# Kernel tuning notes

Measured on AMD Instinct MI355X. Metric: run time of the kernel, lower is better.

Reference implementation:

```python
import jax, jax.numpy as jnp
import numpy as np

N = 50000   # nodes
E = 800000  # edges
IN, HID, HEADS, OUT = 128, 32, 4, 64
NEG_SLOPE = 0.2


def _gatv2_layer(x, src, dst, Wl, bl, Wr, br, att, bias, res_W, concat):
    """One PyG-style GATv2Conv layer (eval mode, no dropout).
    x: [N, F_in]; att: [H, C]. Returns [N, H*C] if concat else [N, C]."""
    H, C = att.shape
    xl = (x @ Wl + bl).reshape(N, H, C)   # source transform
    xr = (x @ Wr + br).reshape(N, H, C)   # target transform
    e = jax.nn.leaky_relu(xl[src] + xr[dst], NEG_SLOPE)        # [E, H, C]
    logit = jnp.einsum('ehc,hc->eh', e, att)                   # [E, H]
    # segment softmax over incoming edges per destination node
    m = jax.ops.segment_max(logit, dst, num_segments=N)        # [N, H]
    p = jnp.exp(logit - m[dst])
    denom = jax.ops.segment_sum(p, dst, num_segments=N)
    alpha = p / (denom[dst] + 1e-16)                           # [E, H]
    out = jax.ops.segment_sum(xl[src] * alpha[:, :, None], dst, num_segments=N)  # [N, H, C]
    out = out.reshape(N, H * C) if concat else out.mean(axis=1)
    if res_W is not None:
        out = out + x @ res_W
    return out + bias


def _glorot(key, shape):
    fan_in = shape[0] if len(shape) > 1 else shape[-1]
    return jax.random.normal(key, shape, dtype=jnp.float32) / np.sqrt(fan_in)


def setup_inputs() -> dict:
    key = jax.random.key(0)
    ks = iter(jax.random.split(key, 32))
    x = jax.random.normal(next(ks), (N, IN), dtype=jnp.float32)
    edge_index = jax.random.randint(next(ks), (2, E), 0, N, dtype=jnp.int64)
    d = {"x": x, "edge_index": edge_index}
    HC = HEADS * HID  # 128
    # layer 0: IN -> HEADS*HID, concat, residual
    d["Wl0"] = _glorot(next(ks), (IN, HC)); d["bl0"] = jnp.zeros((HC,), jnp.float32)
    d["Wr0"] = _glorot(next(ks), (IN, HC)); d["br0"] = jnp.zeros((HC,), jnp.float32)
    d["att0"] = _glorot(next(ks), (HEADS, HID)); d["b0"] = jnp.zeros((HC,), jnp.float32)
    d["res0"] = _glorot(next(ks), (IN, HC))
    # layer 1: HC -> HEADS*HID, concat, residual
    d["Wl1"] = _glorot(next(ks), (HC, HC)); d["bl1"] = jnp.zeros((HC,), jnp.float32)
    d["Wr1"] = _glorot(next(ks), (HC, HC)); d["br1"] = jnp.zeros((HC,), jnp.float32)
    d["att1"] = _glorot(next(ks), (HEADS, HID)); d["b1"] = jnp.zeros((HC,), jnp.float32)
    d["res1"] = _glorot(next(ks), (HC, HC))
    # layer 2: HC -> OUT, heads=1, concat=False, no residual
    d["Wl2"] = _glorot(next(ks), (HC, OUT)); d["bl2"] = jnp.zeros((OUT,), jnp.float32)
    d["Wr2"] = _glorot(next(ks), (HC, OUT)); d["br2"] = jnp.zeros((OUT,), jnp.float32)
    d["att2"] = _glorot(next(ks), (1, OUT)); d["b2"] = jnp.zeros((OUT,), jnp.float32)
    return d


def reference(x, edge_index,
              Wl0, bl0, Wr0, br0, att0, b0, res0,
              Wl1, bl1, Wr1, br1, att1, b1, res1,
              Wl2, bl2, Wr2, br2, att2, b2):
    src, dst = edge_index[0], edge_index[1]
    h = _gatv2_layer(x, src, dst, Wl0, bl0, Wr0, br0, att0, b0, res0, True)
    h = jax.nn.elu(h)
    h = _gatv2_layer(h, src, dst, Wl1, bl1, Wr1, br1, att1, b1, res1, True)
    h = jax.nn.elu(h)
    return _gatv2_layer(h, src, dst, Wl2, bl2, Wr2, br2, att2, b2, None, False)
```

## Files before the change

kernel.cpp:

```cpp
#include <hip/hip_runtime.h>
#include <math.h>

#define NN 50000
#define EE 800000
#define NBK 196
#define EPB 4096

typedef short v8s __attribute__((ext_vector_type(8)));
typedef float v4f __attribute__((ext_vector_type(4)));
typedef float v16f __attribute__((ext_vector_type(16)));

__device__ __forceinline__ ushort f2bf(float f) {
    uint u = __float_as_uint(f);
    uint r = (u + 0x7fffu + ((u >> 16) & 1u)) >> 16;
    return (ushort)r;
}
__device__ __forceinline__ float bf2f(ushort h) {
    return __uint_as_float(((uint)h) << 16);
}
__device__ __forceinline__ float lrelu(float x) {
    return fmaf(0.4f, fabsf(x), 0.6f * x);
}

template <int CTRL>
__device__ __forceinline__ float dppadd(float x) {
    int y = __builtin_amdgcn_update_dpp(0, __float_as_int(x), CTRL, 0xf, 0xf, true);
    return x + __int_as_float(y);
}
__device__ __forceinline__ float sum8(float x) {
    x = dppadd<0xB1>(x);
    x = dppadd<0x4E>(x);
    x = dppadd<0x141>(x);
    return x;
}
__device__ __forceinline__ float sum16(float x) {
    x = sum8(x);
    x = dppadd<0x140>(x);
    return x;
}
__device__ __forceinline__ float expclamp(float t) {
    return __expf(fminf(fmaxf(t, -60.f), 80.f));
}

struct WPack {
    const float* W[8];
    ushort* Th[8];
    ushort* Tl[8];
    int fout[8];
};

__global__ __launch_bounds__(256) void k_build1(const int* __restrict__ edst,
                                                int* __restrict__ bcnt,
                                                WPack p) {
    int t = threadIdx.x;
    if (blockIdx.x < 196) {
        __shared__ int h[NBK];
        if (t < NBK) h[t] = 0;
        __syncthreads();
        int eb = blockIdx.x * EPB;
        #pragma unroll
        for (int k = 0; k < EPB / 256; ++k) {
            int e = eb + k * 256 + t;
            if (e < EE) atomicAdd(&h[edst[e] >> 8], 1);
        }
        __syncthreads();
        if (t < NBK && h[t]) atomicAdd(&bcnt[t], h[t]);
    } else {
        int bid = blockIdx.x - 196;
        int wi = bid >> 6;
        int ib = bid & 63;
        int fout = p.fout[wi];
        int total = 128 * fout;
        int i = ib * 256 + t;
        if (i >= total) return;
        int k = i / fout;
        int n = i - k * fout;
        float f = p.W[wi][i];
        ushort h = f2bf(f);
        float lo = f - bf2f(h);
        int tt = n >> 5, c32 = n & 31, c = k >> 4, khalf = (k >> 3) & 1, j = k & 7;
        int flat = (((tt * 8 + c) * 64) + khalf * 32 + c32) * 8 + j;
        p.Th[wi][flat] = h;
        p.Tl[wi][flat] = f2bf(lo);
    }
}

__global__ __launch_bounds__(256) void k_bktplace(const int* __restrict__ esrc,
                                                  const int* __restrict__ edst,
                                                  const int* __restrict__ bcnt,
                                                  int* __restrict__ gcur,
                                                  uint* __restrict__ ebuf) {
    __shared__ int sc[256];
    __shared__ int h[NBK];
    __shared__ int base[NBK];
    int t = threadIdx.x;
    int v = (t < NBK) ? bcnt[t] : 0;
    sc[t] = v;
    __syncthreads();
    for (int o = 1; o < 256; o <<= 1) {
        int a = (t >= o) ? sc[t - o] : 0;
        __syncthreads();
        sc[t] += a;
        __syncthreads();
    }
    int bexcl = sc[t] - v;
    if (t < NBK) h[t] = 0;
    __syncthreads();

    int eb = blockIdx.x * EPB;
    int pk[EPB / 256];
    #pragma unroll
    for (int k = 0; k < EPB / 256; ++k) {
        int e = eb + k * 256 + t;
        pk[k] = -1;
        if (e < EE) {
            int b = edst[e] >> 8;
            int r = atomicAdd(&h[b], 1);
            pk[k] = (b << 16) | r;
        }
    }
    __syncthreads();
    if (t < NBK && h[t]) base[t] = bexcl + atomicAdd(&gcur[t], h[t]);
    __syncthreads();
    #pragma unroll
    for (int k = 0; k < EPB / 256; ++k) {
        int e = eb + k * 256 + t;
        if (e < EE) {
            int b = pk[k] >> 16;
            int r = pk[k] & 0xFFFF;
            uint dl = (uint)(edst[e] & 255);
            ebuf[base[b] + r] = (dl << 16) | (uint)esrc[e];
        }
    }
}

__global__ __launch_bounds__(256) void k_bktfin(const uint* __restrict__ ebuf,
                                                const int* __restrict__ bcnt,
                                                int* __restrict__ rowptr,
                                                int* __restrict__ csrc) {
    __shared__ int sm[256];
    __shared__ int deg[256];
    __shared__ int cur[256];
    __shared__ int s_eb, s_ec;
    const int b = blockIdx.x;
    const int t = threadIdx.x;

    int v = (t < NBK) ? bcnt[t] : 0;
    sm[t] = v;
    deg[t] = 0;
    __syncthreads();
    for (int o = 1; o < 256; o <<= 1) {
        int a = (t >= o) ? sm[t - o] : 0;
        __syncthreads();
        sm[t] += a;
        __syncthreads();
    }
    if (t == b) { s_eb = sm[t] - v; s_ec = v; }
    __syncthreads();
    const int eb = s_eb;
    const int ec = s_ec;

    for (int k = t; k < ec; k += 256)
        atomicAdd(&deg[ebuf[eb + k] >> 16], 1);
    __syncthreads();
    int dv = deg[t];
    sm[t] = dv;
    __syncthreads();
    for (int o = 1; o < 256; o <<= 1) {
        int a = (t >= o) ? sm[t - o] : 0;
        __syncthreads();
        sm[t] += a;
        __syncthreads();
    }
    int node = b * 256 + t;
    if (node < NN) rowptr[node + 1] = eb + sm[t];
    if (node == 0) rowptr[0] = 0;
    cur[t] = sm[t] - dv;
    __syncthreads();
    for (int k = t; k < ec; k += 256) {
        uint u = ebuf[eb + k];
        int nl = (int)(u >> 16);
        int r = atomicAdd(&cur[nl], 1);
        csrc[eb + r] = (int)(u & 0xFFFFu);
    }
}

template <int FOUT, int NW, bool CVT>
__global__ __launch_bounds__(64) void k_gemm_mfma(
    const float* __restrict__ Xf,
    const ushort* __restrict__ Xh, const ushort* __restrict__ Xl,
    const ushort* __restrict__ T0h, const ushort* __restrict__ T0l, const float* __restrict__ B0,
    const ushort* __restrict__ T1h, const ushort* __restrict__ T1l, const float* __restrict__ B1,
    const ushort* __restrict__ T2h, const ushort* __restrict__ T2l,
    ushort* __restrict__ O0b, float* __restrict__ O1, float* __restrict__ O2)
{
    const int lane  = threadIdx.x & 63;
    const int c32   = lane & 31;
    const int khalf = lane >> 5;
    const int row0  = blockIdx.x * 32;

    const ushort* Th[3] = {T0h, T1h, T2h};
    const ushort* Tl[3] = {T0l, T1l, T2l};
    const float*  Bp[3] = {B0, B1, nullptr};

    v8s ah[8], al[8];
    {
        int arow = row0 + c32;
        if (arow > NN - 1) arow = NN - 1;
        #pragma unroll
        for (int c = 0; c < 8; ++c) {
            size_t off = (size_t)arow * 128 + c * 16 + khalf * 8;
            if constexpr (CVT) {
                float4 f0 = *(const float4*)(Xf + off);
                float4 f1 = *(const float4*)(Xf + off + 4);
                const float fe[8] = {f0.x, f0.y, f0.z, f0.w, f1.x, f1.y, f1.z, f1.w};
                #pragma unroll
                for (int e = 0; e < 8; ++e) {
                    ushort h = f2bf(fe[e]);
                    float lo = fe[e] - bf2f(h);
                    ah[c][e] = (short)h;
                    al[c][e] = (short)(__float_as_uint(lo) >> 16);
                }
            } else {
                ah[c] = *(const v8s*)(Xh + off);
                al[c] = *(const v8s*)(Xl + off);
            }
        }
    }

    #pragma unroll
    for (int w = 0; w < NW; ++w) {
        const ushort* th = Th[w];
        const ushort* tl = Tl[w];
        const float* bias = Bp[w];
        float* Of = (w == 1) ? O1 : O2;
        #pragma unroll
        for (int t = 0; t < FOUT / 32; ++t) {
            v16f acc = {0.f,0.f,0.f,0.f, 0.f,0.f,0.f,0.f, 0.f,0.f,0.f,0.f, 0.f,0.f,0.f,0.f};
            #pragma unroll
            for (int c = 0; c < 8; ++c) {
                int boff = ((t * 8 + c) * 64 + lane) * 8;
                v8s bh = *(const v8s*)(th + boff);
                v8s bl = *(const v8s*)(tl + boff);
                acc = __builtin_amdgcn_mfma_f32_32x32x16_bf16(al[c], bh, acc, 0, 0, 0);
                acc = __builtin_amdgcn_mfma_f32_32x32x16_bf16(ah[c], bl, acc, 0, 0, 0);
                acc = __builtin_amdgcn_mfma_f32_32x32x16_bf16(ah[c], bh, acc, 0, 0, 0);
            }
            const int col = t * 32 + c32;
            float badd = bias ? bias[col] : 0.f;
            if (w == 0) {
                #pragma unroll
                for (int reg = 0; reg < 16; ++reg) {
                    int r = row0 + (reg & 3) + 8 * (reg >> 2) + 4 * khalf;
                    if (r < NN) O0b[(size_t)r * FOUT + col] = f2bf(acc[reg] + badd);
                }
            } else {
                #pragma unroll
                for (int reg = 0; reg < 16; ++reg) {
                    int r = row0 + (reg & 3) + 8 * (reg >> 2) + 4 * khalf;
                    if (r < NN) Of[(size_t)r * FOUT + col] = acc[reg] + badd;
                }
            }
        }
    }
}

__global__ __launch_bounds__(256) void k_agg01(const ushort* __restrict__ XLb,
                                               const float4* __restrict__ XR4,
                                               const float4* __restrict__ RES4,
                                               const float* __restrict__ att,
                                               const float* __restrict__ bias,
                                               const int* __restrict__ rowptr,
                                               const int* __restrict__ csrc,
                                               ushort* __restrict__ Hh,
                                               ushort* __restrict__ Hl) {
    const int lane = threadIdx.x & 63;
    const int wid = threadIdx.x >> 6;
    const int n = blockIdx.x * 4 + wid;
    if (n >= NN) return;
    const int beg = rowptr[n];
    const int end = rowptr[n + 1];
    const int half = lane >> 5;
    const uint j = lane & 31;

    const float4 xr = XR4[(uint)n * 32u + j];
    const float4 at = ((const float4*)att)[j];
    float4 s = {0.f, 0.f, 0.f, 0.f};
    float d = 0.f;

    int i = beg;
    for (; i + 4 <= end; i += 4) {
        uint sa = (uint)csrc[i + half];
        uint sb = (uint)csrc[i + 2 + half];
        ushort4 ua = *(const ushort4*)(XLb + sa * 128u + 4u * j);
        ushort4 ub = *(const ushort4*)(XLb + sb * 128u + 4u * j);
        {
            float4 va = {bf2f(ua.x), bf2f(ua.y), bf2f(ua.z), bf2f(ua.w)};
            float t0 = lrelu(va.x + xr.x) * at.x;
            t0 = fmaf(lrelu(va.y + xr.y), at.y, t0);
            t0 = fmaf(lrelu(va.z + xr.z), at.z, t0);
            t0 = fmaf(lrelu(va.w + xr.w), at.w, t0);
            float p = expclamp(sum8(t0));
            d += p;
            s.x = fmaf(p, va.x, s.x); s.y = fmaf(p, va.y, s.y);
            s.z = fmaf(p, va.z, s.z); s.w = fmaf(p, va.w, s.w);
        }
        {
            float4 vb = {bf2f(ub.x), bf2f(ub.y), bf2f(ub.z), bf2f(ub.w)};
            float t0 = lrelu(vb.x + xr.x) * at.x;
            t0 = fmaf(lrelu(vb.y + xr.y), at.y, t0);
            t0 = fmaf(lrelu(vb.z + xr.z), at.z, t0);
            t0 = fmaf(lrelu(vb.w + xr.w), at.w, t0);
            float p = expclamp(sum8(t0));
            d += p;
            s.x = fmaf(p, vb.x, s.x); s.y = fmaf(p, vb.y, s.y);
            s.z = fmaf(p, vb.z, s.z); s.w = fmaf(p, vb.w, s.w);
        }
    }
    for (; i < end; i += 2) {
        int ia = i + half;
        if (ia > end - 1) ia = end - 1;
        uint sa = (uint)csrc[ia];
        ushort4 ua = *(const ushort4*)(XLb + sa * 128u + 4u * j);
        float4 va = {bf2f(ua.x), bf2f(ua.y), bf2f(ua.z), bf2f(ua.w)};
        float t0 = lrelu(va.x + xr.x) * at.x;
        t0 = fmaf(lrelu(va.y + xr.y), at.y, t0);
        t0 = fmaf(lrelu(va.z + xr.z), at.z, t0);
        t0 = fmaf(lrelu(va.w + xr.w), at.w, t0);
        float p = expclamp(sum8(t0));
        if (half && (i + 1 >= end)) p = 0.f;
        d += p;
        s.x = fmaf(p, va.x, s.x); s.y = fmaf(p, va.y, s.y);
        s.z = fmaf(p, va.z, s.z); s.w = fmaf(p, va.w, s.w);
    }

    d   += __shfl_xor(d, 32);
    s.x += __shfl_xor(s.x, 32);
    s.y += __shfl_xor(s.y, 32);
    s.z += __shfl_xor(s.z, 32);
    s.w += __shfl_xor(s.w, 32);

    if (half == 0) {
        float inv = (d > 0.f) ? 1.f / d : 0.f;
        float4 rv = RES4[(uint)n * 32u + j];
        float4 bv = ((const float4*)bias)[j];
        float o0 = fmaf(s.x, inv, rv.x + bv.x);
        float o1 = fmaf(s.y, inv, rv.y + bv.y);
        float o2 = fmaf(s.z, inv, rv.z + bv.z);
        float o3 = fmaf(s.w, inv, rv.w + bv.w);
        o0 = o0 > 0.f ? o0 : __expf(o0) - 1.f;
        o1 = o1 > 0.f ? o1 : __expf(o1) - 1.f;
        o2 = o2 > 0.f ? o2 : __expf(o2) - 1.f;
        o3 = o3 > 0.f ? o3 : __expf(o3) - 1.f;
        ushort4 h, l;
        h.x = f2bf(o0); l.x = f2bf(o0 - bf2f(h.x));
        h.y = f2bf(o1); l.y = f2bf(o1 - bf2f(h.y));
        h.z = f2bf(o2); l.z = f2bf(o2 - bf2f(h.z));
        h.w = f2bf(o3); l.w = f2bf(o3 - bf2f(h.w));
        *(ushort4*)(Hh + (uint)n * 128u + 4u * j) = h;
        *(ushort4*)(Hl + (uint)n * 128u + 4u * j) = l;
    }
}

__global__ __launch_bounds__(256) void k_agg2(const ushort* __restrict__ XLb,
                                              const float4* __restrict__ XR4,
                                              const float* __restrict__ att,
                                              const float* __restrict__ bias,
                                              const int* __restrict__ rowptr,
                                              const int* __restrict__ csrc,
                                              float* __restrict__ OUT) {
    const int lane = threadIdx.x & 63;
    const int wid = threadIdx.x >> 6;
    const int n = blockIdx.x * 4 + wid;
    if (n >= NN) return;
    const int beg = rowptr[n];
    const int end = rowptr[n + 1];
    const int q = lane >> 4;
    const uint jj = lane & 15;

    const float4 xr = XR4[(uint)n * 16u + jj];
    const float4 at = ((const float4*)att)[jj];
    float4 s = {0.f, 0.f, 0.f, 0.f};
    float d = 0.f;
    const int e1 = end - 1;

    for (int i = beg; i < end; i += 8) {
        int i0 = i + q;
        int i1 = i + 4 + q;
        uint s0 = (uint)csrc[min(i0, e1)];
        uint s1 = (uint)csrc[min(i1, e1)];
        ushort4 u0 = *(const ushort4*)(XLb + s0 * 64u + 4u * jj);
        ushort4 u1 = *(const ushort4*)(XLb + s1 * 64u + 4u * jj);
        #pragma unroll
        for (int u = 0; u < 2; ++u) {
            ushort4 uv = (u == 0) ? u0 : u1;
            int ii = (u == 0) ? i0 : i1;
            float4 v = {bf2f(uv.x), bf2f(uv.y), bf2f(uv.z), bf2f(uv.w)};
            float t0 = lrelu(v.x + xr.x) * at.x;
            t0 = fmaf(lrelu(v.y + xr.y), at.y, t0);
            t0 = fmaf(lrelu(v.z + xr.z), at.z, t0);
            t0 = fmaf(lrelu(v.w + xr.w), at.w, t0);
            float p = expclamp(sum16(t0));
            if (ii >= end) p = 0.f;
            d += p;
            s.x = fmaf(p, v.x, s.x); s.y = fmaf(p, v.y, s.y);
            s.z = fmaf(p, v.z, s.z); s.w = fmaf(p, v.w, s.w);
        }
    }

    d   += __shfl_xor(d, 16);   d   += __shfl_xor(d, 32);
    s.x += __shfl_xor(s.x, 16); s.x += __shfl_xor(s.x, 32);
    s.y += __shfl_xor(s.y, 16); s.y += __shfl_xor(s.y, 32);
    s.z += __shfl_xor(s.z, 16); s.z += __shfl_xor(s.z, 32);
    s.w += __shfl_xor(s.w, 16); s.w += __shfl_xor(s.w, 32);

    if (lane < 16) {
        float inv = (d > 0.f) ? 1.f / d : 0.f;
        float4 bv = ((const float4*)bias)[jj];
        float4 o;
        o.x = fmaf(s.x, inv, bv.x);
        o.y = fmaf(s.y, inv, bv.y);
        o.z = fmaf(s.z, inv, bv.z);
        o.w = fmaf(s.w, inv, bv.w);
        *(float4*)(OUT + (uint)n * 64u + 4u * jj) = o;
    }
}

extern "C" void kernel_launch(void* const* d_in, const int* in_sizes, int n_in,
                              void* d_out, int out_size, void* d_ws, size_t ws_size,
                              hipStream_t stream) {
    const float* x    = (const float*)d_in[0];
    const int*   ei   = (const int*)d_in[1];
    const int*   esrc = ei;
    const int*   edst = ei + EE;

    const float* Wl0 = (const float*)d_in[2];
    const float* bl0 = (const float*)d_in[3];
    const float* Wr0 = (const float*)d_in[4];
    const float* br0 = (const float*)d_in[5];
    const float* at0 = (const float*)d_in[6];
    const float* b0  = (const float*)d_in[7];
    const float* rs0 = (const float*)d_in[8];
    const float* Wl1 = (const float*)d_in[9];
    const float* bl1 = (const float*)d_in[10];
    const float* Wr1 = (const float*)d_in[11];
    const float* br1 = (const float*)d_in[12];
    const float* at1 = (const float*)d_in[13];
    const float* b1  = (const float*)d_in[14];
    const float* rs1 = (const float*)d_in[15];
    const float* Wl2 = (const float*)d_in[16];
    const float* bl2 = (const float*)d_in[17];
    const float* Wr2 = (const float*)d_in[18];
    const float* br2 = (const float*)d_in[19];
    const float* at2 = (const float*)d_in[20];
    const float* b2  = (const float*)d_in[21];

    float* out = (float*)d_out;

    ushort* XLb = (ushort*)d_ws;
    float* XR  = (float*)(XLb + (size_t)NN * 128);
    float* RES = XR + (size_t)NN * 128;
    ushort* Xh = (ushort*)(RES + (size_t)NN * 128);
    ushort* Xl_ = Xh + (size_t)NN * 128;
    ushort* Wth = Xl_ + (size_t)NN * 128;
    const int wsz[8] = {16384, 16384, 16384, 16384, 16384, 16384, 8192, 8192};
    ushort* th[8]; ushort* tl[8];
    {
        ushort* p = Wth;
        for (int i = 0; i < 8; ++i) { th[i] = p; p += wsz[i]; }
        for (int i = 0; i < 8; ++i) { tl[i] = p; p += wsz[i]; }
    }
    int* bcnt   = (int*)(Wth + 2 * (6 * 16384 + 2 * 8192));
    int* gcur   = bcnt + 256;
    int* rowptr = gcur + 256;
    int* csrc   = rowptr + (NN + 1);
    uint* ebuf  = (uint*)(csrc + EE);

    WPack wp;
    const float* Ws[8] = {Wl0, Wr0, rs0, Wl1, Wr1, rs1, Wl2, Wr2};
    const int fouts[8] = {128, 128, 128, 128, 128, 128, 64, 64};
    for (int i = 0; i < 8; ++i) { wp.W[i] = Ws[i]; wp.Th[i] = th[i]; wp.Tl[i] = tl[i]; wp.fout[i] = fouts[i]; }

    hipMemsetAsync(bcnt, 0, 512 * sizeof(int), stream);
    k_build1<<<196 + 512, 256, 0, stream>>>(edst, bcnt, wp);
    k_bktplace<<<196, 256, 0, stream>>>(esrc, edst, bcnt, gcur, ebuf);
    k_bktfin<<<NBK, 256, 0, stream>>>(ebuf, bcnt, rowptr, csrc);

    const int gemm_gx = (NN + 31) / 32;
    const int agg_grid = (NN + 3) / 4;

    k_gemm_mfma<128, 3, true><<<gemm_gx, 64, 0, stream>>>(x, nullptr, nullptr,
        th[0], tl[0], bl0, th[1], tl[1], br0, th[2], tl[2], XLb, XR, RES);
    k_agg01<<<agg_grid, 256, 0, stream>>>(XLb, (const float4*)XR, (const float4*)RES,
        at0, b0, rowptr, csrc, Xh, Xl_);

    k_gemm_mfma<128, 3, false><<<gemm_gx, 64, 0, stream>>>(nullptr, Xh, Xl_,
        th[3], tl[3], bl1, th[4], tl[4], br1, th[5], tl[5], XLb, XR, RES);
    k_agg01<<<agg_grid, 256, 0, stream>>>(XLb, (const float4*)XR, (const float4*)RES,
        at1, b1, rowptr, csrc, Xh, Xl_);

    k_gemm_mfma<64, 2, false><<<gemm_gx, 64, 0, stream>>>(nullptr, Xh, Xl_,
        th[6], tl[6], bl2, th[7], tl[7], br2, nullptr, nullptr, XLb, XR, nullptr);
    k_agg2<<<agg_grid, 256, 0, stream>>>(XLb, (const float4*)XR, at2, b2, rowptr, csrc, out);
}
```

Before: 375.6 us.

## Switch GEMM to 16x16x32 MFMA with 4-wave blocks and weight-grid split

The projection GEMM moves from the 32x32x16 bf16 MFMA on a single 64-thread wave to the 16x16x32 MFMA, with four waves per block each taking 16 rows. The weight matrices are now split across grid y instead of being looped over inside one block. The weight repack layout changes to match the new B-fragment ordering. Two accumulators break the MFMA dependency chain. The aim is more parallelism and occupancy, in exchange for reloading or reconverting the A tile once per weight matrix.

New measurement: 370.0 us. No clear change (-1.5%).

```diff
diff --git a/kernel.cpp b/kernel.cpp
--- a/kernel.cpp
+++ b/kernel.cpp
@@ -8,7 +8,6 @@
 
 typedef short v8s __attribute__((ext_vector_type(8)));
 typedef float v4f __attribute__((ext_vector_type(4)));
-typedef float v16f __attribute__((ext_vector_type(16)));
 
 __device__ __forceinline__ ushort f2bf(float f) {
     uint u = __float_as_uint(f);
@@ -78,8 +77,8 @@
         float f = p.W[wi][i];
         ushort h = f2bf(f);
         float lo = f - bf2f(h);
-        int tt = n >> 5, c32 = n & 31, c = k >> 4, khalf = (k >> 3) & 1, j = k & 7;
-        int flat = (((tt * 8 + c) * 64) + khalf * 32 + c32) * 8 + j;
+        int tt = n >> 4, m = n & 15, c = k >> 5, quad = (k >> 3) & 3, j = k & 7;
+        int flat = ((((tt * 4 + c) * 4 + quad) * 16 + m) << 3) + j;
         p.Th[wi][flat] = h;
         p.Tl[wi][flat] = f2bf(lo);
     }
@@ -185,8 +184,8 @@
     }
 }
 
-template <int FOUT, int NW, bool CVT>
-__global__ __launch_bounds__(64) void k_gemm_mfma(
+template <int FOUT, bool CVT>
+__global__ __launch_bounds__(256) void k_gemm_mfma(
     const float* __restrict__ Xf,
     const ushort* __restrict__ Xh, const ushort* __restrict__ Xl,
     const ushort* __restrict__ T0h, const ushort* __restrict__ T0l, const float* __restrict__ B0,
@@ -194,22 +193,28 @@
     const ushort* __restrict__ T2h, const ushort* __restrict__ T2l,
     ushort* __restrict__ O0b, float* __restrict__ O1, float* __restrict__ O2)
 {
-    const int lane  = threadIdx.x & 63;
-    const int c32   = lane & 31;
-    const int khalf = lane >> 5;
-    const int row0  = blockIdx.x * 32;
+    const int lane = threadIdx.x & 63;
+    const int wid  = threadIdx.x >> 6;
+    const int m    = lane & 15;
+    const int quad = lane >> 4;
+    const int row0 = blockIdx.x * 64 + wid * 16;
+    const int w    = blockIdx.y;
 
     const ushort* Th[3] = {T0h, T1h, T2h};
     const ushort* Tl[3] = {T0l, T1l, T2l};
     const float*  Bp[3] = {B0, B1, nullptr};
-
-    v8s ah[8], al[8];
+    const ushort* th = Th[w];
+    const ushort* tl = Tl[w];
+    const float* bias = Bp[w];
+    float* Of = (w == 1) ? O1 : O2;
+
+    v8s ah[4], al[4];
     {
-        int arow = row0 + c32;
+        int arow = row0 + m;
         if (arow > NN - 1) arow = NN - 1;
         #pragma unroll
-        for (int c = 0; c < 8; ++c) {
-            size_t off = (size_t)arow * 128 + c * 16 + khalf * 8;
+        for (int c = 0; c < 4; ++c) {
+            size_t off = (size_t)arow * 128 + c * 32 + quad * 8;
             if constexpr (CVT) {
                 float4 f0 = *(const float4*)(Xf + off);
                 float4 f1 = *(const float4*)(Xf + off + 4);
@@ -229,37 +234,40 @@
     }
 
     #pragma unroll
-    for (int w = 0; w < NW; ++w) {
-        const ushort* th = Th[w];
-        const ushort* tl = Tl[w];
-        const float* bias = Bp[w];
-        float* Of = (w == 1) ? O1 : O2;
+    for (int t = 0; t < FOUT / 16; ++t) {
+        v4f acc0 = {0.f, 0.f, 0.f, 0.f};
+        v4f acc1 = {0.f, 0.f, 0.f, 0.f};
         #pragma unroll
-        for (int t = 0; t < FOUT / 32; ++t) {
-            v16f acc = {0.f,0.f,0.f,0.f, 0.f,0.f,0.f,0.f, 0.f,0.f,0.f,0.f, 0.f,0.f,0.f,0.f};
+        for (int c = 0; c < 2; ++c) {
+            int boff = t * 2048 + (c * 4 + quad) * 128 + m * 8;
+            v8s bh = *(const v8s*)(th + boff);
+            v8s bl = *(const v8s*)(tl + boff);
+            acc0 = __builtin_amdgcn_mfma_f32_16x16x32_bf16(al[c], bh, acc0, 0, 0, 0);
+            acc0 = __builtin_amdgcn_mfma_f32_16x16x32_bf16(ah[c], bl, acc0, 0, 0, 0);
+            acc0 = __builtin_amdgcn_mfma_f32_16x16x32_bf16(ah[c], bh, acc0, 0, 0, 0);
+        }
+        #pragma unroll
+        for (int c = 2; c < 4; ++c) {
+            int boff = t * 2048 + (c * 4 + quad) * 128 + m * 8;
+            v8s bh = *(const v8s*)(th + boff);
+            v8s bl = *(const v8s*)(tl + boff);
+            acc1 = __builtin_amdgcn_mfma_f32_16x16x32_bf16(al[c], bh, acc1, 0, 0, 0);
+            acc1 = __builtin_amdgcn_mfma_f32_16x16x32_bf16(ah[c], bl, acc1, 0, 0, 0);
+            acc1 = __builtin_amdgcn_mfma_f32_16x16x32_bf16(ah[c], bh, acc1, 0, 0, 0);
+        }
+        const int col = t * 16 + m;
+        float badd = bias ? bias[col] : 0.f;
+        if (w == 0) {
             #pragma unroll
-            for (int c = 0; c < 8; ++c) {
-                int boff = ((t * 8 + c) * 64 + lane) * 8;
-                v8s bh = *(const v8s*)(th + boff);
-                v8s bl = *(const v8s*)(tl + boff);
-                acc = __builtin_amdgcn_mfma_f32_32x32x16_bf16(al[c], bh, acc, 0, 0, 0);
-                acc = __builtin_amdgcn_mfma_f32_32x32x16_bf16(ah[c], bl, acc, 0, 0, 0);
-                acc = __builtin_amdgcn_mfma_f32_32x32x16_bf16(ah[c], bh, acc, 0, 0, 0);
+            for (int j = 0; j < 4; ++j) {
+                int r = row0 + quad * 4 + j;
+                if (r < NN) O0b[(size_t)r * FOUT + col] = f2bf(acc0[j] + acc1[j] + badd);
             }
-            const int col = t * 32 + c32;
-            float badd = bias ? bias[col] : 0.f;
-            if (w == 0) {
-                #pragma unroll
-                for (int reg = 0; reg < 16; ++reg) {
-                    int r = row0 + (reg & 3) + 8 * (reg >> 2) + 4 * khalf;
-                    if (r < NN) O0b[(size_t)r * FOUT + col] = f2bf(acc[reg] + badd);
-                }
-            } else {
-                #pragma unroll
-                for (int reg = 0; reg < 16; ++reg) {
-                    int r = row0 + (reg & 3) + 8 * (reg >> 2) + 4 * khalf;
-                    if (r < NN) Of[(size_t)r * FOUT + col] = acc[reg] + badd;
-                }
+        } else {
+            #pragma unroll
+            for (int j = 0; j < 4; ++j) {
+                int r = row0 + quad * 4 + j;
+                if (r < NN) Of[(size_t)r * FOUT + col] = acc0[j] + acc1[j] + badd;
             }
         }
     }
@@ -486,20 +494,20 @@
     k_bktplace<<<196, 256, 0, stream>>>(esrc, edst, bcnt, gcur, ebuf);
     k_bktfin<<<NBK, 256, 0, stream>>>(ebuf, bcnt, rowptr, csrc);
 
-    const int gemm_gx = (NN + 31) / 32;
+    const int gemm_gx = (NN + 63) / 64;
     const int agg_grid = (NN + 3) / 4;
 
-    k_gemm_mfma<128, 3, true><<<gemm_gx, 64, 0, stream>>>(x, nullptr, nullptr,
+    k_gemm_mfma<128, true><<<dim3(gemm_gx, 3), 256, 0, stream>>>(x, nullptr, nullptr,
         th[0], tl[0], bl0, th[1], tl[1], br0, th[2], tl[2], XLb, XR, RES);
     k_agg01<<<agg_grid, 256, 0, stream>>>(XLb, (const float4*)XR, (const float4*)RES,
         at0, b0, rowptr, csrc, Xh, Xl_);
 
-    k_gemm_mfma<128, 3, false><<<gemm_gx, 64, 0, stream>>>(nullptr, Xh, Xl_,
+    k_gemm_mfma<128, false><<<dim3(gemm_gx, 3), 256, 0, stream>>>(nullptr, Xh, Xl_,
         th[3], tl[3], bl1, th[4], tl[4], br1, th[5], tl[5], XLb, XR, RES);
     k_agg01<<<agg_grid, 256, 0, stream>>>(XLb, (const float4*)XR, (const float4*)RES,
         at1, b1, rowptr, csrc, Xh, Xl_);
 
-    k_gemm_mfma<64, 2, false><<<gemm_gx, 64, 0, stream>>>(nullptr, Xh, Xl_,
+    k_gemm_mfma<64, false><<<dim3(gemm_gx, 2), 256, 0, stream>>>(nullptr, Xh, Xl_,
         th[6], tl[6], bl2, th[7], tl[7], br2, nullptr, nullptr, XLb, XR, nullptr);
     k_agg2<<<agg_grid, 256, 0, stream>>>(XLb, (const float4*)XR, at2, b2, rowptr, csrc, out);
 }
```
